# Kernel optimization log

Measured on AMD Instinct MI355X. Metric: run time of the kernel, lower is better.

## Reference

```python
import jax, jax.numpy as jnp
import numpy as np

B, H, W, C, NH = 128, 14, 14, 768, 12
HD = C // NH  # 64
L = 2 * H - 1  # 27, rel pos table length


def setup_inputs() -> dict:
    key = jax.random.key(0)
    ks = jax.random.split(key, 6)
    return {
        "hidden_states": jax.random.normal(ks[0], (B, H, W, C), jnp.float32),
        "w_qkv": jax.random.normal(ks[1], (C, 3 * C), jnp.float32) * 0.02,
        "b_qkv": jnp.zeros((3 * C,), jnp.float32),
        "rel_pos_h": jax.random.normal(ks[2], (L, HD), jnp.float32) * 0.02,
        "rel_pos_w": jax.random.normal(ks[3], (L, HD), jnp.float32) * 0.02,
        "w_proj": jax.random.normal(ks[4], (C, C), jnp.float32) * 0.02,
        "b_proj": jnp.zeros((C,), jnp.float32),
    }


def _rel_table(size, rel_pos):
    # q_size == k_size -> coords = q - k + (size - 1), pure gather (no resize)
    coords = jnp.arange(size)[:, None] - jnp.arange(size)[None, :] + (size - 1)
    return rel_pos[coords]  # (size, size, HD)


def reference(hidden_states, w_qkv, b_qkv, rel_pos_h, rel_pos_w, w_proj, b_proj):
    scale = HD ** -0.5
    x = hidden_states.reshape(B, H * W, C)
    qkv = x @ w_qkv + b_qkv                                    # (B, HW, 3C)
    qkv = qkv.reshape(B, H * W, 3, NH, HD)
    qkv = jnp.transpose(qkv, (2, 0, 3, 1, 4)).reshape(3, B * NH, H * W, HD)
    q, k, v = qkv[0], qkv[1], qkv[2]                           # (B*NH, HW, HD)

    attn = jnp.einsum('bqd,bkd->bqk', q * scale, k)            # (B*NH, HW, HW)

    Rh = _rel_table(H, rel_pos_h)                              # (H, H, HD)
    Rw = _rel_table(W, rel_pos_w)                              # (W, W, HD)
    qr = q.reshape(B * NH, H, W, HD)
    rel_h = jnp.einsum('bhwc,hkc->bhwk', qr, Rh)               # (B*NH, H, W, H)
    rel_w = jnp.einsum('bhwc,wkc->bhwk', qr, Rw)               # (B*NH, H, W, W)

    attn = attn.reshape(B * NH, H, W, H, W)
    attn = attn + rel_h[..., :, None] + rel_w[..., None, :]
    attn = attn.reshape(B * NH, H * W, H * W)
    attn = jax.nn.softmax(attn, axis=-1)

    out = attn @ v                                             # (B*NH, HW, HD)
    out = out.reshape(B, NH, H, W, HD)
    out = jnp.transpose(out, (0, 2, 3, 1, 4)).reshape(B, H, W, C)
    return out @ w_proj + b_proj
```

## Files before the change

### kernel.cpp

```cpp
#include <hip/hip_runtime.h>

typedef __bf16 bf16_t;
typedef __bf16 bf16x4 __attribute__((ext_vector_type(4)));
typedef __bf16 bf16x8 __attribute__((ext_vector_type(8)));
typedef float floatx4 __attribute__((ext_vector_type(4)));

#define B_    128
#define H_    14
#define HW_   196
#define C_    768
#define NH_   12
#define HD_   64
#define M_    25088
#define NQKV_ 2304
#define KDIM_ 768
#define BK_   64
#define VPAD_ 208
#define RSTR  72
#define QSTR  104
#define PSTR  232

__device__ __forceinline__ void async_cp16(const void* g, void* l) {
    __builtin_amdgcn_global_load_lds((const __attribute__((address_space(1))) void*)g,
                                     (__attribute__((address_space(3))) void*)l, 16, 0, 0);
}

__global__ __launch_bounds__(256) void cast_x_kernel(const float* __restrict__ in,
                                                     bf16_t* __restrict__ out) {
    size_t i = ((size_t)blockIdx.x * 256 + threadIdx.x) * 8;
    float4 a = *(const float4*)(in + i);
    float4 b = *(const float4*)(in + i + 4);
    bf16x8 v;
    v[0] = (bf16_t)a.x; v[1] = (bf16_t)a.y; v[2] = (bf16_t)a.z; v[3] = (bf16_t)a.w;
    v[4] = (bf16_t)b.x; v[5] = (bf16_t)b.y; v[6] = (bf16_t)b.z; v[7] = (bf16_t)b.w;
    *(bf16x8*)(out + i) = v;
}

__global__ __launch_bounds__(256) void zero_vpad_kernel(bf16_t* __restrict__ vtb) {
    int row = blockIdx.x * 256 + threadIdx.x;
    if (row < B_ * NH_ * HD_) {
        bf16_t* p = vtb + (size_t)row * VPAD_ + HW_;
        #pragma unroll
        for (int i = 0; i < 12; i++) p[i] = (bf16_t)0.f;
    }
}

__global__ __launch_bounds__(256) void transpose_cast_kernel(const float* __restrict__ in,
                                                             bf16_t* __restrict__ out,
                                                             int rows, int cols) {
    __shared__ float tile[32][33];
    int c0 = blockIdx.x * 32, r0 = blockIdx.y * 32;
    for (int i = threadIdx.y; i < 32; i += 8) {
        int r = r0 + i, c = c0 + threadIdx.x;
        if (r < rows && c < cols) tile[i][threadIdx.x] = in[(size_t)r * cols + c];
    }
    __syncthreads();
    for (int i = threadIdx.y; i < 32; i += 8) {
        int orow = c0 + i;
        int oc   = r0 + threadIdx.x;
        if (orow < cols && oc < rows)
            out[(size_t)orow * rows + oc] = (bf16_t)tile[threadIdx.x][i];
    }
}

__device__ __forceinline__ void gemm128_compute(const bf16_t* __restrict__ A,
                                                const bf16_t* __restrict__ Bt,
                                                int m0, int n0,
                                                floatx4 acc[4][4],
                                                bf16_t (*As)[BK_], bf16_t (*Bs)[BK_]) {
    const int tid  = threadIdx.x;
    const int lane = tid & 63, wave = tid >> 6;
    const int wm = (wave & 1) << 6, wn = (wave >> 1) << 6;
    const int lrow = lane & 15, quad = lane >> 4;

    #pragma unroll
    for (int i = 0; i < 4; i++)
        #pragma unroll
        for (int j = 0; j < 4; j++) acc[i][j] = (floatx4){0.f, 0.f, 0.f, 0.f};

    const int sr = tid >> 3;
    const int cc = tid & 7;

    for (int k0 = 0; k0 < KDIM_; k0 += BK_) {
        __syncthreads();
        #pragma unroll
        for (int i = 0; i < 4; i++) {
            int row  = sr + i * 32;
            int scol = ((cc ^ (row & 7)) * 8);
            async_cp16(A  + (size_t)(m0 + row) * KDIM_ + k0 + scol, &As[row][cc * 8]);
            async_cp16(Bt + (size_t)(n0 + row) * KDIM_ + k0 + scol, &Bs[row][cc * 8]);
        }
        __syncthreads();

        #pragma unroll
        for (int kh = 0; kh < 2; kh++) {
            bf16x8 af[4], bfr[4];
            #pragma unroll
            for (int i = 0; i < 4; i++) {
                int rw = wm + i * 16 + lrow;
                af[i] = *(const bf16x8*)&As[rw][((kh * 4 + quad) ^ (rw & 7)) * 8];
            }
            #pragma unroll
            for (int j = 0; j < 4; j++) {
                int rw = wn + j * 16 + lrow;
                bfr[j] = *(const bf16x8*)&Bs[rw][((kh * 4 + quad) ^ (rw & 7)) * 8];
            }
            #pragma unroll
            for (int i = 0; i < 4; i++)
                #pragma unroll
                for (int j = 0; j < 4; j++)
                    acc[i][j] = __builtin_amdgcn_mfma_f32_16x16x32_bf16(af[i], bfr[j], acc[i][j], 0, 0, 0);
        }
    }
}

__global__ __launch_bounds__(256) void qkv_gemm_kernel(const bf16_t* __restrict__ A,
                                                       const bf16_t* __restrict__ Bt,
                                                       const float* __restrict__ bias,
                                                       bf16_t* __restrict__ qb,
                                                       bf16_t* __restrict__ kb,
                                                       bf16_t* __restrict__ vtb) {
    __shared__ __align__(16) char smem[128 * 136 * 2];
    bf16_t (*As)[BK_] = (bf16_t(*)[BK_])smem;
    bf16_t (*Bs)[BK_] = (bf16_t(*)[BK_])(smem + 128 * BK_ * 2);
    bf16_t (*Cs)[136] = (bf16_t(*)[136])smem;

    const int lin = blockIdx.x;
    const int g = lin / 72, r = lin - g * 72;
    const int m0 = (g * 4 + (r & 3)) * 128;
    const int n0 = (r >> 2) * 128;
    floatx4 acc[4][4];
    gemm128_compute(A, Bt, m0, n0, acc, As, Bs);

    const int tid = threadIdx.x;
    const int lane = tid & 63, wave = tid >> 6;
    const int wm = (wave & 1) << 6, wn = (wave >> 1) << 6;
    const int lrow = lane & 15, quad = lane >> 4;
    const int sel = n0 / C_;

    if (sel == 2) {
        #pragma unroll
        for (int j = 0; j < 4; j++) {
            int n = n0 + wn + j * 16 + lrow;
            float bv = bias[n];
            int nc = n - 2 * C_;
            int nh = nc >> 6, hd = nc & 63;
            #pragma unroll
            for (int i = 0; i < 4; i++) {
                int m = m0 + wm + i * 16 + quad * 4;
                int b = m / HW_, t = m - b * HW_;
                int head = b * NH_ + nh;
                ushort4 pk;
                bf16_t h;
                h = (bf16_t)(acc[i][j][0] + bv); pk.x = __builtin_bit_cast(unsigned short, h);
                h = (bf16_t)(acc[i][j][1] + bv); pk.y = __builtin_bit_cast(unsigned short, h);
                h = (bf16_t)(acc[i][j][2] + bv); pk.z = __builtin_bit_cast(unsigned short, h);
                h = (bf16_t)(acc[i][j][3] + bv); pk.w = __builtin_bit_cast(unsigned short, h);
                *(ushort4*)(vtb + ((size_t)head * HD_ + hd) * VPAD_ + t) = pk;
            }
        }
    } else {
        const float sc = (sel == 0) ? 0.125f : 1.0f;
        __syncthreads();
        #pragma unroll
        for (int j = 0; j < 4; j++) {
            int n = n0 + wn + j * 16 + lrow;
            float bv = bias[n];
            #pragma unroll
            for (int i = 0; i < 4; i++)
                #pragma unroll
                for (int rr = 0; rr < 4; rr++)
                    Cs[wm + i * 16 + quad * 4 + rr][wn + j * 16 + lrow] =
                        (bf16_t)((acc[i][j][rr] + bv) * sc);
        }
        __syncthreads();
        bf16_t* dst = sel ? kb : qb;
        const int n0s = n0 - sel * C_;
        #pragma unroll
        for (int u = 0; u < 8; u++) {
            int idx = tid + u * 256;
            int rr = idx >> 4, c = idx & 15;
            int m = m0 + rr;
            int b = m / HW_, t = m - b * HW_;
            int ncol = n0s + c * 8;
            int nh = ncol >> 6, hd = ncol & 63;
            *(uint4*)(dst + (((size_t)(b * NH_ + nh)) * HW_ + t) * HD_ + hd) =
                *(const uint4*)&Cs[rr][c * 8];
        }
    }
}

__global__ __launch_bounds__(256) void proj_gemm_kernel(const bf16_t* __restrict__ A,
                                                        const bf16_t* __restrict__ Bt,
                                                        const float* __restrict__ bias,
                                                        float* __restrict__ out) {
    __shared__ __align__(16) bf16_t As[128][BK_];
    __shared__ __align__(16) bf16_t Bs[128][BK_];
    const int lin = blockIdx.x;
    const int g = lin / 24, r = lin - g * 24;
    const int m0 = (g * 4 + (r & 3)) * 128;
    const int n0 = (r >> 2) * 128;
    floatx4 acc[4][4];
    gemm128_compute(A, Bt, m0, n0, acc, As, Bs);

    const int lane = threadIdx.x & 63, wave = threadIdx.x >> 6;
    const int wm = (wave & 1) << 6, wn = (wave >> 1) << 6;
    const int lrow = lane & 15, quad = lane >> 4;
    #pragma unroll
    for (int j = 0; j < 4; j++) {
        int n = n0 + wn + j * 16 + lrow;
        float bv = bias[n];
        #pragma unroll
        for (int i = 0; i < 4; i++) {
            #pragma unroll
            for (int rr = 0; rr < 4; rr++) {
                int m = m0 + wm + i * 16 + quad * 4 + rr;
                out[(size_t)m * C_ + n] = acc[i][j][rr] + bv;
            }
        }
    }
}

__global__ __launch_bounds__(256, 2) void attn_kernel(const bf16_t* __restrict__ qb,
                                                      const bf16_t* __restrict__ kb,
                                                      const bf16_t* __restrict__ vtb,
                                                      const float* __restrict__ rph,
                                                      const float* __restrict__ rpw,
                                                      bf16_t* __restrict__ aout) {
    const int head = blockIdx.x;
    const int bb = head / NH_, nh = head - bb * NH_;
    const int tid = threadIdx.x;
    const int lane = tid & 63, wave = tid >> 6;
    const int lrow = lane & 15, quad = lane >> 4;

    __shared__ __align__(16) bf16_t qs[32][QSTR];
    __shared__ __align__(16) bf16_t ks[208][QSTR];
    __shared__ __align__(16) bf16_t pb[32][PSTR];
    __shared__ __align__(16) bf16_t rT[64][RSTR];
    __shared__ bf16_t QRh[32][34];
    __shared__ bf16_t QRw[32][34];
    __shared__ float pmax[2][32], psum[2][32];

    bf16x8 z;
    #pragma unroll
    for (int e = 0; e < 8; e++) z[e] = (bf16_t)0.f;

    #pragma unroll
    for (int t2 = 0; t2 < 2; t2++) {
        int u = tid * 2 + t2;
        int which = u >> 8, rem = u & 255;
        int l = rem >> 3, c = (rem & 7) * 8;
        bf16x8 v = z;
        if (l < 27) {
            const float* src = (which ? rpw : rph) + (size_t)l * HD_ + c;
            float4 a = *(const float4*)src;
            float4 b = *(const float4*)(src + 4);
            v[0] = (bf16_t)a.x; v[1] = (bf16_t)a.y; v[2] = (bf16_t)a.z; v[3] = (bf16_t)a.w;
            v[4] = (bf16_t)b.x; v[5] = (bf16_t)b.y; v[6] = (bf16_t)b.z; v[7] = (bf16_t)b.w;
        }
        *(bf16x8*)&rT[which * 32 + l][c] = v;
    }
    for (int v8 = tid; v8 < 208 * 8; v8 += 256) {
        int row = v8 >> 3, col = (v8 & 7) * 8;
        *(bf16x8*)&ks[row][col] =
            (row < HW_) ? *(const bf16x8*)(kb + ((size_t)head * HW_ + row) * HD_ + col) : z;
    }
    for (int u = tid; u < 208 * 5; u += 256) {
        int row = u / 5, c = u - row * 5;
        *(bf16x8*)&ks[row][64 + c * 8] = z;
    }

    bf16x8 vfr[2][7];
    #pragma unroll
    for (int jj = 0; jj < 2; jj++) {
        int hdt = (wave >> 1) * 2 + jj;
        #pragma unroll
        for (int kk = 0; kk < 7; kk++) {
            int col = kk * 32 + quad * 8;
            bool ok = (col < VPAD_);
            bf16x8 t = *(const bf16x8*)(vtb + ((size_t)head * HD_ + hdt * 16 + lrow) * VPAD_
                                        + (ok ? col : 0));
            vfr[jj][kk] = ok ? t : z;
        }
    }

    const int qrow_st = tid >> 3, qcol_st = (tid & 7) * 8;
    bf16x8 qreg = *(const bf16x8*)(qb + ((size_t)head * HW_ + qrow_st) * HD_ + qcol_st);

    __syncthreads();
    if (tid < HW_) {
        int kh = tid / 14, kw = tid - kh * 14;
        ks[tid][64 + kh] = (bf16_t)1.0f;
        ks[tid][78 + kw] = (bf16_t)1.0f;
    }
    if (tid < 96) {
        int row = tid / 3, col = 208 + (tid % 3) * 8;
        *(bf16x8*)&pb[row][col] = z;
    }

    const int wh = wave >> 1, mi = wave & 1;
    const int qit = wave & 1;

    for (int qt = 0; qt < 7; qt++) {
        const int q0 = qt * 32;

        *(bf16x8*)&qs[qrow_st][qcol_st] = qreg;
        __syncthreads();

        #pragma unroll
        for (int t2 = 0; t2 < 2; t2++) {
            int tsk = wave * 2 + t2;
            int which = tsk >> 2, mi2 = (tsk >> 1) & 1, ni = tsk & 1;
            floatx4 a4 = (floatx4){0.f, 0.f, 0.f, 0.f};
            #pragma unroll
            for (int kk = 0; kk < 2; kk++) {
                bf16x8 af  = *(const bf16x8*)&qs[mi2 * 16 + lrow][kk * 32 + quad * 8];
                bf16x8 bf8 = *(const bf16x8*)&rT[which * 32 + ni * 16 + lrow][kk * 32 + quad * 8];
                a4 = __builtin_amdgcn_mfma_f32_16x16x32_bf16(af, bf8, a4, 0, 0, 0);
            }
            int l = ni * 16 + lrow;
            if (l < 27) {
                bf16_t (*QR)[34] = which ? QRw : QRh;
                #pragma unroll
                for (int rr = 0; rr < 4; rr++) QR[mi2 * 16 + quad * 4 + rr][l] = (bf16_t)(a4[rr] * 8.f);
            }
        }
        __syncthreads();

        {
            int row = tid >> 3;
            int kk4 = (tid & 7) * 4;
            int t = q0 + row;
            int h = t / 14, w = t - h * 14;
            bf16x4 pk;
            #pragma unroll
            for (int s = 0; s < 4; s++) {
                int kk = kk4 + s;
                bf16_t val = (bf16_t)0.f;
                if (kk < 14)      val = QRh[row][h - kk + 13];
                else if (kk < 28) val = QRw[row][w - (kk - 14) + 13];
                pk[s] = val;
            }
            *(bf16x4*)&qs[row][64 + kk4] = pk;
        }
        __syncthreads();

        float sv[7][4];
        float m4[4] = {-1e30f, -1e30f, -1e30f, -1e30f};
        #pragma unroll
        for (int t = 0; t < 7; t++) {
            int jt = 2 * t + wh;
            if (jt < 13) {
                floatx4 a4 = (floatx4){0.f, 0.f, 0.f, 0.f};
                #pragma unroll
                for (int kk = 0; kk < 3; kk++) {
                    bf16x8 af  = *(const bf16x8*)&qs[mi * 16 + lrow][kk * 32 + quad * 8];
                    bf16x8 bf8 = *(const bf16x8*)&ks[jt * 16 + lrow][kk * 32 + quad * 8];
                    a4 = __builtin_amdgcn_mfma_f32_16x16x32_bf16(af, bf8, a4, 0, 0, 0);
                }
                int n = jt * 16 + lrow;
                bool valid = (n < HW_);
                #pragma unroll
                for (int rr = 0; rr < 4; rr++) {
                    float s = valid ? a4[rr] : -1e30f;
                    sv[t][rr] = s;
                    m4[rr] = fmaxf(m4[rr], s);
                }
            }
        }
        #pragma unroll
        for (int off = 1; off < 16; off <<= 1)
            #pragma unroll
            for (int rr = 0; rr < 4; rr++) m4[rr] = fmaxf(m4[rr], __shfl_xor(m4[rr], off));
        if (lrow == 0)
            #pragma unroll
            for (int rr = 0; rr < 4; rr++) pmax[wh][mi * 16 + quad * 4 + rr] = m4[rr];
        __syncthreads();

        float mxr[4], s4[4] = {0.f, 0.f, 0.f, 0.f};
        #pragma unroll
        for (int rr = 0; rr < 4; rr++) {
            int qi = mi * 16 + quad * 4 + rr;
            mxr[rr] = fmaxf(pmax[0][qi], pmax[1][qi]);
        }
        #pragma unroll
        for (int t = 0; t < 7; t++) {
            int jt = 2 * t + wh;
            if (jt < 13) {
                int n = jt * 16 + lrow;
                #pragma unroll
                for (int rr = 0; rr < 4; rr++) {
                    float e = __expf(sv[t][rr] - mxr[rr]);
                    s4[rr] += e;
                    pb[mi * 16 + quad * 4 + rr][n] = (bf16_t)e;
                }
            }
        }
        #pragma unroll
        for (int off = 1; off < 16; off <<= 1)
            #pragma unroll
            for (int rr = 0; rr < 4; rr++) s4[rr] += __shfl_xor(s4[rr], off);
        if (lrow == 0)
            #pragma unroll
            for (int rr = 0; rr < 4; rr++) psum[wh][mi * 16 + quad * 4 + rr] = s4[rr];
        __syncthreads();

        const int qrow = qit * 16 + lrow;
        const float inv = 1.f / (psum[0][qrow] + psum[1][qrow]);
        const int t_out = q0 + qrow;

        if (qt < 6) {
            int t = q0 + 32 + qrow_st;
            qreg = (t < HW_) ? *(const bf16x8*)(qb + ((size_t)head * HW_ + t) * HD_ + qcol_st) : z;
        }

        #pragma unroll
        for (int jj = 0; jj < 2; jj++) {
            int hdt = (wave >> 1) * 2 + jj;
            floatx4 a4 = (floatx4){0.f, 0.f, 0.f, 0.f};
            #pragma unroll
            for (int kk = 0; kk < 7; kk++) {
                bf16x8 bf8 = *(const bf16x8*)&pb[qit * 16 + lrow][kk * 32 + quad * 8];
                a4 = __builtin_amdgcn_mfma_f32_16x16x32_bf16(vfr[jj][kk], bf8, a4, 0, 0, 0);
            }
            if (t_out < HW_) {
                int col = nh * HD_ + hdt * 16 + quad * 4;
                ushort4 pk;
                bf16_t hv;
                hv = (bf16_t)(a4[0] * inv); pk.x = __builtin_bit_cast(unsigned short, hv);
                hv = (bf16_t)(a4[1] * inv); pk.y = __builtin_bit_cast(unsigned short, hv);
                hv = (bf16_t)(a4[2] * inv); pk.z = __builtin_bit_cast(unsigned short, hv);
                hv = (bf16_t)(a4[3] * inv); pk.w = __builtin_bit_cast(unsigned short, hv);
                *(ushort4*)(aout + ((size_t)bb * HW_ + t_out) * C_ + col) = pk;
            }
        }
    }
}

extern "C" void kernel_launch(void* const* d_in, const int* in_sizes, int n_in,
                              void* d_out, int out_size, void* d_ws, size_t ws_size,
                              hipStream_t stream) {
    const float* hs    = (const float*)d_in[0];
    const float* wqkv  = (const float*)d_in[1];
    const float* bqkv  = (const float*)d_in[2];
    const float* rph   = (const float*)d_in[3];
    const float* rpw   = (const float*)d_in[4];
    const float* wproj = (const float*)d_in[5];
    const float* bproj = (const float*)d_in[6];
    float* out = (float*)d_out;

    char* ws = (char*)d_ws;
    bf16_t* x_bf   = (bf16_t*)(ws + 0);
    bf16_t* aout   = x_bf;
    bf16_t* wqkvT  = (bf16_t*)(ws + 38535168);
    bf16_t* wprojT = (bf16_t*)(ws + 42074112);
    bf16_t* qb     = (bf16_t*)(ws + 43253760);
    bf16_t* kb     = (bf16_t*)(ws + 81788928);
    bf16_t* vtb    = (bf16_t*)(ws + 120324096);

    cast_x_kernel<<<9408, 256, 0, stream>>>(hs, x_bf);
    zero_vpad_kernel<<<384, 256, 0, stream>>>(vtb);
    transpose_cast_kernel<<<dim3(72, 24), dim3(32, 8), 0, stream>>>(wqkv, wqkvT, 768, 2304);
    transpose_cast_kernel<<<dim3(24, 24), dim3(32, 8), 0, stream>>>(wproj, wprojT, 768, 768);
    qkv_gemm_kernel<<<3528, 256, 0, stream>>>(x_bf, wqkvT, bqkv, qb, kb, vtb);
    attn_kernel<<<B_ * NH_, 256, 0, stream>>>(qb, kb, vtb, rph, rpw, aout);
    proj_gemm_kernel<<<1176, 256, 0, stream>>>(aout, wprojT, bproj, out);
}
```

Baseline: 411.0 us.

## Double-buffer LDS tiles in QKV and projection GEMMs to overlap loads with MFMA

Result: no change. 413.1 us (+0.5%).

```diff
diff --git a/kernel.cpp b/kernel.cpp
--- a/kernel.cpp
+++ b/kernel.cpp
@@ -15,6 +15,7 @@
 #define NQKV_ 2304
 #define KDIM_ 768
 #define BK_   64
+#define NKT_  12
 #define VPAD_ 208
 #define RSTR  72
 #define QSTR  104
@@ -63,11 +64,22 @@
     }
 }
 
-__device__ __forceinline__ void gemm128_compute(const bf16_t* __restrict__ A,
-                                                const bf16_t* __restrict__ Bt,
-                                                int m0, int n0,
-                                                floatx4 acc[4][4],
-                                                bf16_t (*As)[BK_], bf16_t (*Bs)[BK_]) {
+__device__ __forceinline__ void stage128(const bf16_t* __restrict__ G, int g0, int kt,
+                                         bf16_t (*Lb)[BK_], int tid) {
+    const int sr = tid >> 3, cc = tid & 7;
+    #pragma unroll
+    for (int i = 0; i < 4; i++) {
+        int row  = sr + i * 32;
+        int scol = ((cc ^ (row & 7)) * 8);
+        async_cp16(G + (size_t)(g0 + row) * KDIM_ + kt * BK_ + scol, &Lb[row][cc * 8]);
+    }
+}
+
+__device__ __forceinline__ void gemm128_pipe(const bf16_t* __restrict__ A,
+                                             const bf16_t* __restrict__ Bt,
+                                             int m0, int n0,
+                                             floatx4 acc[4][4],
+                                             bf16_t (*As)[BK_], bf16_t (*Bs)[BK_]) {
     const int tid  = threadIdx.x;
     const int lane = tid & 63, wave = tid >> 6;
     const int wm = (wave & 1) << 6, wn = (wave >> 1) << 6;
@@ -78,19 +90,22 @@
         #pragma unroll
         for (int j = 0; j < 4; j++) acc[i][j] = (floatx4){0.f, 0.f, 0.f, 0.f};
 
-    const int sr = tid >> 3;
-    const int cc = tid & 7;
-
-    for (int k0 = 0; k0 < KDIM_; k0 += BK_) {
-        __syncthreads();
-        #pragma unroll
-        for (int i = 0; i < 4; i++) {
-            int row  = sr + i * 32;
-            int scol = ((cc ^ (row & 7)) * 8);
-            async_cp16(A  + (size_t)(m0 + row) * KDIM_ + k0 + scol, &As[row][cc * 8]);
-            async_cp16(Bt + (size_t)(n0 + row) * KDIM_ + k0 + scol, &Bs[row][cc * 8]);
-        }
-        __syncthreads();
+    stage128(A,  m0, 0, As, tid);
+    stage128(Bt, n0, 0, Bs, tid);
+
+    for (int kt = 0; kt < NKT_; kt++) {
+        __builtin_amdgcn_sched_barrier(0);
+        asm volatile("s_waitcnt vmcnt(0) lgkmcnt(0)" ::: "memory");
+        __builtin_amdgcn_s_barrier();
+        __builtin_amdgcn_sched_barrier(0);
+
+        bf16_t (*Ab)[BK_] = As + (kt & 1) * 128;
+        bf16_t (*Bb)[BK_] = Bs + (kt & 1) * 128;
+
+        if (kt + 1 < NKT_) {
+            stage128(A,  m0, kt + 1, As + ((kt + 1) & 1) * 128, tid);
+            stage128(Bt, n0, kt + 1, Bs + ((kt + 1) & 1) * 128, tid);
+        }
 
         #pragma unroll
         for (int kh = 0; kh < 2; kh++) {
@@ -98,12 +113,12 @@
             #pragma unroll
             for (int i = 0; i < 4; i++) {
                 int rw = wm + i * 16 + lrow;
-                af[i] = *(const bf16x8*)&As[rw][((kh * 4 + quad) ^ (rw & 7)) * 8];
+                af[i] = *(const bf16x8*)&Ab[rw][((kh * 4 + quad) ^ (rw & 7)) * 8];
             }
             #pragma unroll
             for (int j = 0; j < 4; j++) {
                 int rw = wn + j * 16 + lrow;
-                bfr[j] = *(const bf16x8*)&Bs[rw][((kh * 4 + quad) ^ (rw & 7)) * 8];
+                bfr[j] = *(const bf16x8*)&Bb[rw][((kh * 4 + quad) ^ (rw & 7)) * 8];
             }
             #pragma unroll
             for (int i = 0; i < 4; i++)
@@ -112,6 +127,7 @@
                     acc[i][j] = __builtin_amdgcn_mfma_f32_16x16x32_bf16(af[i], bfr[j], acc[i][j], 0, 0, 0);
         }
     }
+    __syncthreads();
 }
 
 __global__ __launch_bounds__(256) void qkv_gemm_kernel(const bf16_t* __restrict__ A,
@@ -120,9 +136,9 @@
                                                        bf16_t* __restrict__ qb,
                                                        bf16_t* __restrict__ kb,
                                                        bf16_t* __restrict__ vtb) {
-    __shared__ __align__(16) char smem[128 * 136 * 2];
+    __shared__ __align__(16) char smem[65536];
     bf16_t (*As)[BK_] = (bf16_t(*)[BK_])smem;
-    bf16_t (*Bs)[BK_] = (bf16_t(*)[BK_])(smem + 128 * BK_ * 2);
+    bf16_t (*Bs)[BK_] = (bf16_t(*)[BK_])(smem + 32768);
     bf16_t (*Cs)[136] = (bf16_t(*)[136])smem;
 
     const int lin = blockIdx.x;
@@ -130,7 +146,7 @@
     const int m0 = (g * 4 + (r & 3)) * 128;
     const int n0 = (r >> 2) * 128;
     floatx4 acc[4][4];
-    gemm128_compute(A, Bt, m0, n0, acc, As, Bs);
+    gemm128_pipe(A, Bt, m0, n0, acc, As, Bs);
 
     const int tid = threadIdx.x;
     const int lane = tid & 63, wave = tid >> 6;
@@ -161,7 +177,6 @@
         }
     } else {
         const float sc = (sel == 0) ? 0.125f : 1.0f;
-        __syncthreads();
         #pragma unroll
         for (int j = 0; j < 4; j++) {
             int n = n0 + wn + j * 16 + lrow;
@@ -194,14 +209,14 @@
                                                         const bf16_t* __restrict__ Bt,
                                                         const float* __restrict__ bias,
                                                         float* __restrict__ out) {
-    __shared__ __align__(16) bf16_t As[128][BK_];
-    __shared__ __align__(16) bf16_t Bs[128][BK_];
+    __shared__ __align__(16) bf16_t As[256][BK_];
+    __shared__ __align__(16) bf16_t Bs[256][BK_];
     const int lin = blockIdx.x;
     const int g = lin / 24, r = lin - g * 24;
     const int m0 = (g * 4 + (r & 3)) * 128;
     const int n0 = (r >> 2) * 128;
     floatx4 acc[4][4];
-    gemm128_compute(A, Bt, m0, n0, acc, As, Bs);
+    gemm128_pipe(A, Bt, m0, n0, acc, As, Bs);
 
     const int lane = threadIdx.x & 63, wave = threadIdx.x >> 6;
     const int wm = (wave & 1) << 6, wn = (wave >> 1) << 6;
```
